# Optimization experiments

Hardware: AMD Instinct MI355X
Metric: run time of the kernel (lower is better)

The kernel has to match this reference:

```python
import jax, jax.numpy as jnp
import numpy as np

B, N, D, Z, H = 256, 128, 256, 64, 128

def setup_inputs() -> dict:
    key = jax.random.key(0)
    ks = jax.random.split(key, 12)
    s = 0.02
    inp = {
        "h_obs": jax.random.normal(ks[0], (B, N, D), jnp.float32),
        "z": jax.random.normal(ks[1], (B, N, Z), jnp.float32),
        "start_pos": jax.random.normal(ks[2], (B, N, 2), jnp.float32),
        # input_proj: Linear(D+Z+2 -> H)
        "W_in": jax.random.normal(ks[3], (D + Z + 2, H), jnp.float32) * s,
        "b_in": jax.random.normal(ks[4], (H,), jnp.float32) * s,
        # GRUCell weights, PyTorch layout: [3H, H] rows ordered (r, z, n)
        "W_ih": jax.random.normal(ks[5], (3 * H, H), jnp.float32) * s,
        "b_ih": jax.random.normal(ks[6], (3 * H,), jnp.float32) * s,
        "W_hh": jax.random.normal(ks[7], (3 * H, H), jnp.float32) * s,
        "b_hh": jax.random.normal(ks[8], (3 * H,), jnp.float32) * s,
        # out_proj: Linear(H -> 2)
        "W_out": jax.random.normal(ks[9], (2, H), jnp.float32) * s,
        "b_out": jax.random.normal(ks[10], (2,), jnp.float32) * s,
        "pred_len": 30,
    }
    return inp

def _gru_cell(x, h, W_ih, b_ih, W_hh, b_hh):
    gi = x @ W_ih.T + b_ih            # [BN, 3H]
    gh = h @ W_hh.T + b_hh            # [BN, 3H]
    i_r, i_z, i_n = jnp.split(gi, 3, axis=-1)
    h_r, h_z, h_n = jnp.split(gh, 3, axis=-1)
    r = jax.nn.sigmoid(i_r + h_r)
    zg = jax.nn.sigmoid(i_z + h_z)
    n = jnp.tanh(i_n + r * h_n)
    return (1.0 - zg) * n + zg * h

def reference(h_obs, z, start_pos, W_in, b_in, W_ih, b_ih, W_hh, b_hh, W_out, b_out, pred_len):
    BN = B * N
    # h_obs and z are constant across steps: precompute their projection once.
    base = jnp.concatenate([h_obs, z], axis=-1).reshape(BN, D + Z)
    base_proj = base @ W_in[: D + Z] + b_in            # [BN, H]
    W_pos = W_in[D + Z:]                               # [2, H]

    state0 = jnp.zeros((BN, H), h_obs.dtype)
    pos0 = start_pos.reshape(BN, 2)

    def step(carry, _):
        state, pos = carry
        x = base_proj + pos @ W_pos                    # == input_proj(cat(h,z,pos))
        state = _gru_cell(x, state, W_ih, b_ih, W_hh, b_hh)
        delta = state @ W_out.T + b_out                # [BN, 2]
        pos = pos + delta
        return (state, pos), pos

    (_, _), traj = jax.lax.scan(step, (state0, pos0), None, length=pred_len)
    # traj: [T, BN, 2] -> [B, T, N, 2]
    return traj.reshape(pred_len, B, N, 2).transpose(1, 0, 2, 3)
```

## Files before the change

kernel.cpp:

```cpp
#include <hip/hip_runtime.h>
#include <hip/hip_bf16.h>


#define T_LEN 30
#define H_    128
#define G3_   384
#define KIN_  320
#define S2B   272
#define HB    (64*S2B)
#define TRAJ_OFF (2*HB)
#define LDS_BYTES (TRAJ_OFF + T_LEN*64*8)

#define SCL_RZ -1.44269504088896341f
#define SCL_N   2.88539008177792681f

typedef float  f32x4 __attribute__((ext_vector_type(4)));
typedef __bf16 b16x8 __attribute__((ext_vector_type(8)));
typedef unsigned u32x4 __attribute__((ext_vector_type(4)));

#define MFMA16(a,b,c) __builtin_amdgcn_mfma_f32_16x16x32_bf16((a),(b),(c),0,0,0)

__device__ __forceinline__ b16x8 pack8s(const float* p, float s){
  b16x8 r;
  #pragma unroll
  for (int i=0;i<8;i++) r[i] = (__bf16)(s*p[i]);
  return r;
}
__device__ __forceinline__ unsigned pk2(float a, float b){
  __bf16 x=(__bf16)a, y=(__bf16)b;
  unsigned short ux=__builtin_bit_cast(unsigned short,x);
  unsigned short uy=__builtin_bit_cast(unsigned short,y);
  return (unsigned)ux | ((unsigned)uy<<16);
}
__device__ __forceinline__ f32x4 unpk2(unsigned lo, unsigned hi){
  f32x4 r;
  r[0]=__builtin_bit_cast(float, lo<<16);
  r[1]=__builtin_bit_cast(float, lo&0xFFFF0000u);
  r[2]=__builtin_bit_cast(float, hi<<16);
  r[3]=__builtin_bit_cast(float, hi&0xFFFF0000u);
  return r;
}
__device__ __forceinline__ b16x8 fragu(unsigned v){
  u32x4 t = {v,0u,0u,0u};
  return __builtin_bit_cast(b16x8, t);
}

__global__ void prep_wc(const float* __restrict__ W_in, const float* __restrict__ W_ih,
                        __bf16* __restrict__ WcT){
  __shared__ float win[H_][16];
  int k0 = blockIdx.x << 4;
  for (int i=threadIdx.x; i<16*H_; i+=384){
    int kk = i>>7, m = i&127;
    win[m][kk] = W_in[(size_t)(k0+kk)*H_ + m];
  }
  __syncthreads();
  int j = threadIdx.x;
  const float* wr = W_ih + (size_t)j*H_;
  float acc[16];
  #pragma unroll
  for (int kk=0;kk<16;kk++) acc[kk]=0.f;
  for (int m=0;m<H_;m++){
    float wv = wr[m];
    #pragma unroll
    for (int kk=0;kk<16;kk++) acc[kk] = fmaf(wv, win[m][kk], acc[kk]);
  }
  float scl = (j < 2*H_) ? SCL_RZ : SCL_N;
  #pragma unroll
  for (int kk=0;kk<16;kk++) WcT[(size_t)j*KIN_ + k0 + kk] = (__bf16)(scl*acc[kk]);
}

__global__ void prep_vec(const float* __restrict__ W_in, const float* __restrict__ b_in,
                         const float* __restrict__ W_ih, const float* __restrict__ b_ih,
                         const float* __restrict__ b_hh, const float* __restrict__ b_out,
                         float* __restrict__ cvec, float* __restrict__ P2G){
  int j = threadIdx.x;
  const float* wr = W_ih + (size_t)j*H_;
  float s  = b_ih[j] + (j < 2*H_ ? b_hh[j] : 0.f);
  float p0 = 0.f, p1 = 0.f;
  #pragma unroll 8
  for (int m=0;m<H_;m++){
    float wv = wr[m];
    s  += b_in[m]*wv;
    p0 += W_in[(size_t)KIN_*H_ + m]*wv;
    p1 += W_in[(size_t)(KIN_+1)*H_ + m]*wv;
  }
  float scl = (j < 2*H_) ? SCL_RZ : SCL_N;
  float p0s = scl*p0, p1s = scl*p1;
  P2G[j] = p0s; P2G[G3_ + j] = p1s;
  cvec[j] = scl*s + b_out[0]*p0s + b_out[1]*p1s;
}

__global__ void prep_wt(const float* __restrict__ W_hh, const float* __restrict__ W_out,
                        const float* __restrict__ P2G, __bf16* __restrict__ WT){
  int jp = blockIdx.x;
  int set = jp >> 7, col = jp & 127;
  int j = (set==0) ? col : (set==1) ? H_+col : 2*H_+col;
  float p0 = P2G[j], p1 = P2G[G3_+j];
  int k = threadIdx.x;
  if (k >= 136) return;
  float v = 0.f;
  if (k < 128){
    if (set<=1)      v = SCL_RZ*W_hh[(size_t)j*H_+k] + p0*W_out[k] + p1*W_out[H_+k];
    else if (set==2) v = SCL_N *W_hh[(size_t)j*H_+k];
    else             v = p0*W_out[k] + p1*W_out[H_+k];
  } else if (k==128){ v = (set==2)? 0.f : p0; }
  else if (k==129){ v = (set==2)? 0.f : p1; }
  WT[(size_t)jp*136 + k] = (__bf16)v;
}

__global__ __launch_bounds__(512, 2)
void decoder(const float* __restrict__ h_obs, const float* __restrict__ zin,
             const float* __restrict__ start_pos,
             const float* __restrict__ b_hh, const float* __restrict__ W_out,
             const float* __restrict__ b_out,
             const __bf16* __restrict__ WcT, const float* __restrict__ cvec,
             const __bf16* __restrict__ WT, float* __restrict__ out)
{
  __shared__ __align__(16) char lds[LDS_BYTES];
  __bf16* stg = (__bf16*)lds;

  const int tid  = threadIdx.x;
  const int lane = tid & 63;
  const int w    = tid >> 6;
  const int l15  = lane & 15;
  const int lhi  = lane >> 4;
  const int R0   = blockIdx.x << 6;
  const int hcol = (w<<4) + l15;
  const int jr = hcol, jz = H_ + hcol, jn = 2*H_ + hcol;
  const int oc = l15 & 1;
  const bool desig = (w < 4);
  const int gd = w >> 1, md = w & 1;

  {
    const float4* src = reinterpret_cast<const float4*>(h_obs) + (size_t)R0*64;
    #pragma unroll
    for (int i=0;i<8;i++){
      int k = tid + (i<<9);
      float4 v = src[k];
      int r = k>>6, c = (k&63)<<2;
      __bf16* d = &stg[r*328 + c];
      d[0]=(__bf16)v.x; d[1]=(__bf16)v.y; d[2]=(__bf16)v.z; d[3]=(__bf16)v.w;
    }
    const float4* srcz = reinterpret_cast<const float4*>(zin) + (size_t)R0*16;
    #pragma unroll
    for (int i=0;i<2;i++){
      int k = tid + (i<<9);
      float4 v = srcz[k];
      int r = k>>4, c = 256 + ((k&15)<<2);
      __bf16* d = &stg[r*328 + c];
      d[0]=(__bf16)v.x; d[1]=(__bf16)v.y; d[2]=(__bf16)v.z; d[3]=(__bf16)v.w;
    }
  }

  const float bo0 = b_out[0], bo1 = b_out[1];
  const float bo  = oc ? bo1 : bo0;
  const float bhn = SCL_N * b_hh[2*H_ + hcol];
  const f32x4 bhnvec = (f32x4){bhn,bhn,bhn,bhn};
  const f32x4 bovec  = (f32x4){bo,bo,bo,bo};

  float px[4]={0,0,0,0}, py[4]={0,0,0,0};
  if (desig){
    #pragma unroll
    for (int q=0;q<4;q++){
      int r = R0 + (gd<<5) + (md<<4) + (lhi<<2) + q;
      px[q] = start_pos[2*r]   - bo0;
      py[q] = start_pos[2*r+1] - bo1;
    }
  }

  __syncthreads();

  f32x4 G[2][3][2];
  {
    float cr = cvec[jr], cz = cvec[jz], cn = cvec[jn];
    #pragma unroll
    for (int g=0; g<2; g++){
      G[g][0][0] = (f32x4){cr,cr,cr,cr}; G[g][0][1] = G[g][0][0];
      G[g][1][0] = (f32x4){cz,cz,cz,cz}; G[g][1][1] = G[g][1][0];
      G[g][2][0] = (f32x4){cn,cn,cn,cn}; G[g][2][1] = G[g][2][0];
    }
    #pragma unroll 1
    for (int kk=0; kk<10; kk++){
      const int ko = (kk<<5) + (lhi<<3);
      b16x8 br = *reinterpret_cast<const b16x8*>(WcT + (size_t)jr*KIN_ + ko);
      b16x8 bz = *reinterpret_cast<const b16x8*>(WcT + (size_t)jz*KIN_ + ko);
      b16x8 bn = *reinterpret_cast<const b16x8*>(WcT + (size_t)jn*KIN_ + ko);
      #pragma unroll
      for (int g=0; g<2; g++){
        b16x8 a0 = *reinterpret_cast<const b16x8*>(&stg[(g*32   +l15)*328 + ko]);
        b16x8 a1 = *reinterpret_cast<const b16x8*>(&stg[(g*32+16+l15)*328 + ko]);
        G[g][0][0] = MFMA16(a0, br, G[g][0][0]); G[g][0][1] = MFMA16(a1, br, G[g][0][1]);
        G[g][1][0] = MFMA16(a0, bz, G[g][1][0]); G[g][1][1] = MFMA16(a1, bz, G[g][1][1]);
        G[g][2][0] = MFMA16(a0, bn, G[g][2][0]); G[g][2][1] = MFMA16(a1, bn, G[g][2][1]);
      }
    }
  }

  b16x8 Br[4],Bz[4],Ban[4],Binn[4],Bo[4];
  #pragma unroll
  for (int kk=0;kk<4;kk++){
    const int ko = kk*32 + lhi*8;
    Br[kk]   = *reinterpret_cast<const b16x8*>(WT + (size_t)(      hcol)*136 + ko);
    Bz[kk]   = *reinterpret_cast<const b16x8*>(WT + (size_t)(128 + hcol)*136 + ko);
    Ban[kk]  = *reinterpret_cast<const b16x8*>(WT + (size_t)(256 + hcol)*136 + ko);
    Binn[kk] = *reinterpret_cast<const b16x8*>(WT + (size_t)(384 + hcol)*136 + ko);
    Bo[kk]   = pack8s(W_out + (size_t)oc*H_ + ko, 1.0f);
  }
  const b16x8 Br4 = fragu(lhi==0 ? *reinterpret_cast<const unsigned*>(WT + (size_t)(      hcol)*136 + 128) : 0u);
  const b16x8 Bz4 = fragu(lhi==0 ? *reinterpret_cast<const unsigned*>(WT + (size_t)(128 + hcol)*136 + 128) : 0u);
  const b16x8 Bi4 = fragu(lhi==0 ? *reinterpret_cast<const unsigned*>(WT + (size_t)(384 + hcol)*136 + 128) : 0u);

  __syncthreads();

  for (int i=tid; i<4096; i+=512){
    int r = i>>6, dw = i&63;
    *reinterpret_cast<unsigned*>(lds + r*S2B + dw*4) = 0u;
  }
  if (desig && l15==0){
    #pragma unroll
    for (int q=0;q<4;q++){
      int row = (gd<<5) + (md<<4) + (lhi<<2) + q;
      *reinterpret_cast<unsigned*>(lds + row*S2B + 256) = pk2(px[q], py[q]);
    }
  }

  unsigned stp[2][2][2];
  #pragma unroll
  for (int g=0;g<2;g++)
    #pragma unroll
    for (int m=0;m<2;m++){ stp[g][m][0]=0u; stp[g][m][1]=0u; }

  const unsigned rdb = (unsigned)(l15*S2B + lhi*16);

  int cur = 0;
  #pragma unroll 1
  for (int t=0; t<T_LEN; ++t){
    __syncthreads();
    const char* rb = lds + cur*HB;
    char*       wb = lds + (cur^1)*HB;

    #pragma unroll
    for (int g=0; g<2; ++g){
      const char* rg_ = rb + g*(32*S2B);
      char*       wg_ = wb + g*(32*S2B);

      f32x4 ar0 = G[g][0][0], ar1 = G[g][0][1];
      f32x4 az0 = G[g][1][0], az1 = G[g][1][1];
      f32x4 ai0 = G[g][2][0], ai1 = G[g][2][1];
      f32x4 an0 = bhnvec, an1 = bhnvec;

      #pragma unroll
      for (int kk=0;kk<4;kk++){
        b16x8 a0 = *reinterpret_cast<const b16x8*>(rg_ + rdb + kk*64);
        b16x8 a1 = *reinterpret_cast<const b16x8*>(rg_ + rdb + 16*S2B + kk*64);
        ar0 = MFMA16(a0,Br[kk],ar0);   ar1 = MFMA16(a1,Br[kk],ar1);
        az0 = MFMA16(a0,Bz[kk],az0);   az1 = MFMA16(a1,Bz[kk],az1);
        an0 = MFMA16(a0,Ban[kk],an0);  an1 = MFMA16(a1,Ban[kk],an1);
        ai0 = MFMA16(a0,Binn[kk],ai0); ai1 = MFMA16(a1,Binn[kk],ai1);
      }
      {
        unsigned pp0 = *reinterpret_cast<const unsigned*>(rg_ + l15*S2B + 256);
        unsigned pp1 = *reinterpret_cast<const unsigned*>(rg_ + (16+l15)*S2B + 256);
        b16x8 a40 = fragu(lhi==0 ? pp0 : 0u);
        b16x8 a41 = fragu(lhi==0 ? pp1 : 0u);
        ar0 = MFMA16(a40,Br4,ar0); ar1 = MFMA16(a41,Br4,ar1);
        az0 = MFMA16(a40,Bz4,az0); az1 = MFMA16(a41,Bz4,az1);
        ai0 = MFMA16(a40,Bi4,ai0); ai1 = MFMA16(a41,Bi4,ai1);
      }

      if (desig && gd == g){
        f32x4 d = bovec;
        if (md==0){
          #pragma unroll
          for (int kk=0;kk<4;kk++){
            b16x8 fk = *reinterpret_cast<const b16x8*>(rg_ + rdb + kk*64);
            d = MFMA16(fk,Bo[kk],d);
          }
        } else {
          #pragma unroll
          for (int kk=0;kk<4;kk++){
            b16x8 fk = *reinterpret_cast<const b16x8*>(rg_ + rdb + 16*S2B + kk*64);
            d = MFMA16(fk,Bo[kk],d);
          }
        }
        #pragma unroll
        for (int q=0;q<4;q++){
          float dme  = d[q];
          float doth = __shfl_xor(dme, 1);
          px[q] += oc ? doth : dme;
          py[q] += oc ? dme  : doth;
        }
        if (l15==0){
          #pragma unroll
          for (int q=0;q<4;q++){
            int row = (gd<<5) + (md<<4) + (lhi<<2) + q;
            if (t > 0){
              float2 v; v.x = px[q]; v.y = py[q];
              *reinterpret_cast<float2*>(lds + TRAJ_OFF + ((t-1)*64 + row)*8) = v;
            }
            *reinterpret_cast<unsigned*>(wb + row*S2B + 256) = pk2(px[q], py[q]);
          }
        }
      }

      #pragma unroll
      for (int m=0;m<2;m++){
        f32x4 Ar = m? ar1:ar0, Az = m? az1:az0, An = m? an1:an0, Ai = m? ai1:ai0;
        f32x4 stv = unpk2(stp[g][m][0], stp[g][m][1]);
        float hq[4];
        #pragma unroll
        for (int q=0;q<4;q++){
          float rgt = __builtin_amdgcn_rcpf(1.f + __builtin_amdgcn_exp2f(Ar[q]));
          float zgt = __builtin_amdgcn_rcpf(1.f + __builtin_amdgcn_exp2f(Az[q]));
          float na  = fmaf(rgt, An[q], Ai[q]);
          float nn  = fmaf(-2.f, __builtin_amdgcn_rcpf(1.f + __builtin_amdgcn_exp2f(na)), 1.f);
          float h   = fmaf(zgt, stv[q] - nn, nn);
          hq[q] = h;
          *reinterpret_cast<__bf16*>(wg_ + ((m<<4)+(lhi<<2)+q)*S2B + hcol*2) = (__bf16)h;
        }
        stp[g][m][0] = pk2(hq[0], hq[1]);
        stp[g][m][1] = pk2(hq[2], hq[3]);
      }
    }
    cur ^= 1;
  }

  __syncthreads();
  if (desig){
    const char* rg_ = lds + cur*HB + gd*(32*S2B);
    const unsigned dbase = (unsigned)((md*16 + l15)*S2B + lhi*16);
    f32x4 d = bovec;
    #pragma unroll
    for (int kk=0;kk<4;kk++){
      b16x8 fk = *reinterpret_cast<const b16x8*>(rg_ + dbase + kk*64);
      d = MFMA16(fk, Bo[kk], d);
    }
    #pragma unroll
    for (int q=0;q<4;q++){
      float dme  = d[q];
      float doth = __shfl_xor(dme, 1);
      px[q] += oc ? doth : dme;
      py[q] += oc ? dme  : doth;
    }
    if (l15==0){
      #pragma unroll
      for (int q=0;q<4;q++){
        int row = (gd<<5) + (md<<4) + (lhi<<2) + q;
        float2 v; v.x = px[q]; v.y = py[q];
        *reinterpret_cast<float2*>(lds + TRAJ_OFF + ((T_LEN-1)*64 + row)*8) = v;
      }
    }
  }

  __syncthreads();
  {
    const float* trajf = reinterpret_cast<const float*>(lds + TRAJ_OFF);
    const size_t ob  = ((size_t)(R0>>7)*T_LEN)<<8;
    const int    n02 = (R0 & 127)<<1;
    for (int i=tid; i<T_LEN*128; i+=512){
      int tt = i>>7, j = i&127;
      out[ob + (size_t)tt*256 + n02 + j] = trajf[i];
    }
  }
}

extern "C" void kernel_launch(void* const* d_in, const int* in_sizes, int n_in,
                              void* d_out, int out_size, void* d_ws, size_t ws_size,
                              hipStream_t stream) {
  const float* h_obs     = (const float*)d_in[0];
  const float* z         = (const float*)d_in[1];
  const float* start_pos = (const float*)d_in[2];
  const float* W_in      = (const float*)d_in[3];
  const float* b_in      = (const float*)d_in[4];
  const float* W_ih      = (const float*)d_in[5];
  const float* b_ih      = (const float*)d_in[6];
  const float* W_hh      = (const float*)d_in[7];
  const float* b_hh      = (const float*)d_in[8];
  const float* W_out     = (const float*)d_in[9];
  const float* b_out     = (const float*)d_in[10];

  char* ws = (char*)d_ws;
  __bf16* WcT  = (__bf16*)ws;
  float*  cvec = (float*)(ws + 245760);
  float*  P2G  = (float*)(ws + 247296);
  __bf16* WT   = (__bf16*)(ws + 250368);

  prep_wc <<<20,  384, 0, stream>>>(W_in, W_ih, WcT);
  prep_vec<<<1,   384, 0, stream>>>(W_in, b_in, W_ih, b_ih, b_hh, b_out, cvec, P2G);
  prep_wt <<<512, 192, 0, stream>>>(W_hh, W_out, P2G, WT);
  decoder <<<512, 512, 0, stream>>>(h_obs, z, start_pos, b_hh, W_out, b_out,
                                    WcT, cvec, WT, (float*)d_out);
}
```

Measured before the change: 295.2 us.

## Use current position directly instead of folding W_out into gate weights

Before, the position update was folded algebraically into the gate weight matrices, which cost an extra fourth weight set (Binn) and 8 more MFMAs per group. Now the step computes delta first, writes the new position to a small LDS buffer, then applies the pos-to-gate projection from that updated position after an added barrier. The delta MFMA now shares the A fragments of the main loop. This drops MFMAs and registers but adds a second __syncthreads per timestep on the serial critical path.

```diff
diff --git a/kernel.cpp b/kernel.cpp
--- a/kernel.cpp
+++ b/kernel.cpp
@@ -9,7 +9,8 @@
 #define S2B   272
 #define HB    (64*S2B)
 #define TRAJ_OFF (2*HB)
-#define LDS_BYTES (TRAJ_OFF + T_LEN*64*8)
+#define POS_OFF  (TRAJ_OFF + T_LEN*64*8)
+#define LDS_BYTES (POS_OFF + 256)
 
 #define SCL_RZ -1.44269504088896341f
 #define SCL_N   2.88539008177792681f
@@ -85,9 +86,8 @@
     p1 += W_in[(size_t)(KIN_+1)*H_ + m]*wv;
   }
   float scl = (j < 2*H_) ? SCL_RZ : SCL_N;
-  float p0s = scl*p0, p1s = scl*p1;
-  P2G[j] = p0s; P2G[G3_ + j] = p1s;
-  cvec[j] = scl*s + b_out[0]*p0s + b_out[1]*p1s;
+  P2G[j] = scl*p0; P2G[G3_ + j] = scl*p1;
+  cvec[j] = scl*s;
 }
 
 __global__ void prep_wt(const float* __restrict__ W_hh, const float* __restrict__ W_out,
@@ -100,9 +100,9 @@
   if (k >= 136) return;
   float v = 0.f;
   if (k < 128){
-    if (set<=1)      v = SCL_RZ*W_hh[(size_t)j*H_+k] + p0*W_out[k] + p1*W_out[H_+k];
-    else if (set==2) v = SCL_N *W_hh[(size_t)j*H_+k];
-    else             v = p0*W_out[k] + p1*W_out[H_+k];
+    if (set==0 || set==1) v = SCL_RZ*W_hh[(size_t)j*H_+k];
+    else if (set==2)      v = SCL_N *W_hh[(size_t)j*H_+k];
+    else                  v = 0.f;
   } else if (k==128){ v = (set==2)? 0.f : p0; }
   else if (k==129){ v = (set==2)? 0.f : p1; }
   WT[(size_t)jp*136 + k] = (__bf16)v;
@@ -196,14 +196,13 @@
     }
   }
 
-  b16x8 Br[4],Bz[4],Ban[4],Binn[4],Bo[4];
+  b16x8 Br[4],Bz[4],Ban[4],Bo[4];
   #pragma unroll
   for (int kk=0;kk<4;kk++){
     const int ko = kk*32 + lhi*8;
     Br[kk]   = *reinterpret_cast<const b16x8*>(WT + (size_t)(      hcol)*136 + ko);
     Bz[kk]   = *reinterpret_cast<const b16x8*>(WT + (size_t)(128 + hcol)*136 + ko);
     Ban[kk]  = *reinterpret_cast<const b16x8*>(WT + (size_t)(256 + hcol)*136 + ko);
-    Binn[kk] = *reinterpret_cast<const b16x8*>(WT + (size_t)(384 + hcol)*136 + ko);
     Bo[kk]   = pack8s(W_out + (size_t)oc*H_ + ko, 1.0f);
   }
   const b16x8 Br4 = fragu(lhi==0 ? *reinterpret_cast<const unsigned*>(WT + (size_t)(      hcol)*136 + 128) : 0u);
@@ -215,13 +214,6 @@
   for (int i=tid; i<4096; i+=512){
     int r = i>>6, dw = i&63;
     *reinterpret_cast<unsigned*>(lds + r*S2B + dw*4) = 0u;
-  }
-  if (desig && l15==0){
-    #pragma unroll
-    for (int q=0;q<4;q++){
-      int row = (gd<<5) + (md<<4) + (lhi<<2) + q;
-      *reinterpret_cast<unsigned*>(lds + row*S2B + 256) = pk2(px[q], py[q]);
-    }
   }
 
   unsigned stp[2][2][2];
@@ -239,16 +231,16 @@
     const char* rb = lds + cur*HB;
     char*       wb = lds + (cur^1)*HB;
 
+    f32x4 AR[2][2], AZ[2][2], AN[2][2];
+
     #pragma unroll
     for (int g=0; g<2; ++g){
       const char* rg_ = rb + g*(32*S2B);
-      char*       wg_ = wb + g*(32*S2B);
-
+      const bool own = (desig && gd == g);
       f32x4 ar0 = G[g][0][0], ar1 = G[g][0][1];
       f32x4 az0 = G[g][1][0], az1 = G[g][1][1];
-      f32x4 ai0 = G[g][2][0], ai1 = G[g][2][1];
-      f32x4 an0 = bhnvec, an1 = bhnvec;
-
+      f32x4 an0 = bhnvec,     an1 = bhnvec;
+      f32x4 dAcc = bovec;
       #pragma unroll
       for (int kk=0;kk<4;kk++){
         b16x8 a0 = *reinterpret_cast<const b16x8*>(rg_ + rdb + kk*64);
@@ -256,36 +248,12 @@
         ar0 = MFMA16(a0,Br[kk],ar0);   ar1 = MFMA16(a1,Br[kk],ar1);
         az0 = MFMA16(a0,Bz[kk],az0);   az1 = MFMA16(a1,Bz[kk],az1);
         an0 = MFMA16(a0,Ban[kk],an0);  an1 = MFMA16(a1,Ban[kk],an1);
-        ai0 = MFMA16(a0,Binn[kk],ai0); ai1 = MFMA16(a1,Binn[kk],ai1);
-      }
-      {
-        unsigned pp0 = *reinterpret_cast<const unsigned*>(rg_ + l15*S2B + 256);
-        unsigned pp1 = *reinterpret_cast<const unsigned*>(rg_ + (16+l15)*S2B + 256);
-        b16x8 a40 = fragu(lhi==0 ? pp0 : 0u);
-        b16x8 a41 = fragu(lhi==0 ? pp1 : 0u);
-        ar0 = MFMA16(a40,Br4,ar0); ar1 = MFMA16(a41,Br4,ar1);
-        az0 = MFMA16(a40,Bz4,az0); az1 = MFMA16(a41,Bz4,az1);
-        ai0 = MFMA16(a40,Bi4,ai0); ai1 = MFMA16(a41,Bi4,ai1);
-      }
-
-      if (desig && gd == g){
-        f32x4 d = bovec;
-        if (md==0){
-          #pragma unroll
-          for (int kk=0;kk<4;kk++){
-            b16x8 fk = *reinterpret_cast<const b16x8*>(rg_ + rdb + kk*64);
-            d = MFMA16(fk,Bo[kk],d);
-          }
-        } else {
-          #pragma unroll
-          for (int kk=0;kk<4;kk++){
-            b16x8 fk = *reinterpret_cast<const b16x8*>(rg_ + rdb + 16*S2B + kk*64);
-            d = MFMA16(fk,Bo[kk],d);
-          }
-        }
+        if (own){ b16x8 am = md ? a1 : a0; dAcc = MFMA16(am, Bo[kk], dAcc); }
+      }
+      if (own){
         #pragma unroll
         for (int q=0;q<4;q++){
-          float dme  = d[q];
+          float dme  = dAcc[q];
           float doth = __shfl_xor(dme, 1);
           px[q] += oc ? doth : dme;
           py[q] += oc ? dme  : doth;
@@ -298,14 +266,31 @@
               float2 v; v.x = px[q]; v.y = py[q];
               *reinterpret_cast<float2*>(lds + TRAJ_OFF + ((t-1)*64 + row)*8) = v;
             }
-            *reinterpret_cast<unsigned*>(wb + row*S2B + 256) = pk2(px[q], py[q]);
+            *reinterpret_cast<unsigned*>(lds + POS_OFF + row*4) = pk2(px[q], py[q]);
           }
         }
       }
-
+      AR[g][0]=ar0; AR[g][1]=ar1;
+      AZ[g][0]=az0; AZ[g][1]=az1;
+      AN[g][0]=an0; AN[g][1]=an1;
+    }
+
+    __syncthreads();
+
+    #pragma unroll
+    for (int g=0; g<2; ++g){
+      char* wg_ = wb + g*(32*S2B);
+      unsigned pp0 = *reinterpret_cast<const unsigned*>(lds + POS_OFF + ((g<<5) + l15)*4);
+      unsigned pp1 = *reinterpret_cast<const unsigned*>(lds + POS_OFF + ((g<<5) + 16 + l15)*4);
+      b16x8 a40 = fragu(lhi==0 ? pp0 : 0u);
+      b16x8 a41 = fragu(lhi==0 ? pp1 : 0u);
+      f32x4 ar0 = MFMA16(a40,Br4,AR[g][0]), ar1 = MFMA16(a41,Br4,AR[g][1]);
+      f32x4 az0 = MFMA16(a40,Bz4,AZ[g][0]), az1 = MFMA16(a41,Bz4,AZ[g][1]);
+      f32x4 ai0 = MFMA16(a40,Bi4,G[g][2][0]), ai1 = MFMA16(a41,Bi4,G[g][2][1]);
       #pragma unroll
       for (int m=0;m<2;m++){
-        f32x4 Ar = m? ar1:ar0, Az = m? az1:az0, An = m? an1:an0, Ai = m? ai1:ai0;
+        f32x4 Ar = m? ar1:ar0, Az = m? az1:az0, Ai = m? ai1:ai0;
+        f32x4 An = AN[g][m];
         f32x4 stv = unpk2(stp[g][m][0], stp[g][m][1]);
         float hq[4];
         #pragma unroll
```

Result: no change. 292.5 us (-0.9%).
